# Performance work log

Hardware: AMD Instinct MI355X
Metric: run time of the kernel (lower is better)

Reference implementation:

```python
import jax, jax.numpy as jnp
import numpy as np

D_MODEL = 1024
N_HEADS = 16
D_K = D_MODEL // N_HEADS
SCALE = float(np.sqrt(D_K))


def depthwise3(x, w, b):
    # x: [B, S, D]; w: [D, 3] (PyTorch Conv1d weight [D,1,3] squeezed); b: [D]
    # cross-correlation with kernel_size=3, padding=1, groups=D
    xp = jnp.pad(x, ((0, 0), (1, 1), (0, 0)))
    return xp[:, :-2] * w[:, 0] + xp[:, 1:-1] * w[:, 1] + xp[:, 2:] * w[:, 2] + b


def setup_inputs() -> dict:
    key = jax.random.key(0)
    ks = jax.random.split(key, 16)
    B, S, D = 2, 2048, D_MODEL
    s_lin = 1.0 / np.sqrt(D)
    s_dw = 1.0 / np.sqrt(3)
    inp = {
        "x": jax.random.normal(ks[0], (B, S, D), dtype=jnp.float32),
        "dwq_w": jax.random.uniform(ks[1], (D, 3), jnp.float32, -s_dw, s_dw),
        "dwq_b": jax.random.uniform(ks[2], (D,), jnp.float32, -s_dw, s_dw),
        "dwk_w": jax.random.uniform(ks[3], (D, 3), jnp.float32, -s_dw, s_dw),
        "dwk_b": jax.random.uniform(ks[4], (D,), jnp.float32, -s_dw, s_dw),
        "dwv_w": jax.random.uniform(ks[5], (D, 3), jnp.float32, -s_dw, s_dw),
        "dwv_b": jax.random.uniform(ks[6], (D,), jnp.float32, -s_dw, s_dw),
        "wq": jax.random.uniform(ks[7], (D, D), jnp.float32, -s_lin, s_lin),
        "bq": jax.random.uniform(ks[8], (D,), jnp.float32, -s_lin, s_lin),
        "wk": jax.random.uniform(ks[9], (D, D), jnp.float32, -s_lin, s_lin),
        "bk": jax.random.uniform(ks[10], (D,), jnp.float32, -s_lin, s_lin),
        "wv": jax.random.uniform(ks[11], (D, D), jnp.float32, -s_lin, s_lin),
        "bv": jax.random.uniform(ks[12], (D,), jnp.float32, -s_lin, s_lin),
        "wo": jax.random.uniform(ks[13], (D, D), jnp.float32, -s_lin, s_lin),
        "bo": jax.random.uniform(ks[14], (D,), jnp.float32, -s_lin, s_lin),
    }
    return inp


def reference(x, dwq_w, dwq_b, dwk_w, dwk_b, dwv_w, dwv_b,
              wq, bq, wk, bk, wv, bv, wo, bo):
    B, S, D = x.shape
    # depthwise conv (k=3, pad=1) then linear projection (PyTorch: y = x @ W^T + b)
    q = depthwise3(x, dwq_w, dwq_b) @ wq.T + bq
    k = depthwise3(x, dwk_w, dwk_b) @ wk.T + bk
    v = depthwise3(x, dwv_w, dwv_b) @ wv.T + bv
    # [B, H, S, d_k]
    q = q.reshape(B, S, N_HEADS, D_K).transpose(0, 2, 1, 3)
    k = k.reshape(B, S, N_HEADS, D_K).transpose(0, 2, 1, 3)
    v = v.reshape(B, S, N_HEADS, D_K).transpose(0, 2, 1, 3)
    scores = jnp.einsum("bhqd,bhkd->bhqk", q, k) / SCALE
    attn = jax.nn.softmax(scores, axis=-1)  # dropout=0 (eval)
    out = jnp.einsum("bhqk,bhkd->bhqd", attn, v)
    out = out.transpose(0, 2, 1, 3).reshape(B, S, D)
    return out @ wo.T + bo
```

## Files before the change

kernel.cpp:

```cpp
#include <hip/hip_runtime.h>

typedef __bf16 bf16x8 __attribute__((ext_vector_type(8)));
typedef float f32x4 __attribute__((ext_vector_type(4)));
typedef float f32x16 __attribute__((ext_vector_type(16)));
typedef unsigned short u16x8 __attribute__((ext_vector_type(8)));
typedef unsigned short u16x4 __attribute__((ext_vector_type(4)));
typedef unsigned int u32x2 __attribute__((ext_vector_type(2)));

__device__ __forceinline__ unsigned short f2bf(float f) {
  union { float f; unsigned int u; } v; v.f = f;
  unsigned int r = v.u + 0x7FFFu + ((v.u >> 16) & 1u);
  return (unsigned short)(r >> 16);
}

__device__ __forceinline__ void gload_lds16(const void* g, void* l) {
  __builtin_amdgcn_global_load_lds(
      (const __attribute__((address_space(1))) void*)g,
      (__attribute__((address_space(3))) void*)l, 16, 0, 0);
}

__global__ __launch_bounds__(256)
void conv3_kernel(const float* __restrict__ x,
                  const float* __restrict__ wq, const float* __restrict__ bq,
                  const float* __restrict__ wk, const float* __restrict__ bk,
                  const float* __restrict__ wv, const float* __restrict__ bv,
                  unsigned short* __restrict__ cq, unsigned short* __restrict__ ck,
                  unsigned short* __restrict__ cv)
{
  int t = blockIdx.x;
  int s = t & 2047;
  int d0 = threadIdx.x * 4;
  int base = t * 1024 + d0;
  f32x4 xc = *(const f32x4*)(x + base);
  f32x4 xm = (s > 0)    ? *(const f32x4*)(x + base - 1024) : f32x4{0.f,0.f,0.f,0.f};
  f32x4 xp = (s < 2047) ? *(const f32x4*)(x + base + 1024) : f32x4{0.f,0.f,0.f,0.f};

  #pragma unroll
  for (int path = 0; path < 3; path++) {
    const float* wP = (path == 0) ? wq : ((path == 1) ? wk : wv);
    const float* bP = (path == 0) ? bq : ((path == 1) ? bk : bv);
    unsigned short* oP = (path == 0) ? cq : ((path == 1) ? ck : cv);
    f32x4 w0 = *(const f32x4*)(wP + d0*3);
    f32x4 w1 = *(const f32x4*)(wP + d0*3 + 4);
    f32x4 w2 = *(const f32x4*)(wP + d0*3 + 8);
    f32x4 b4 = *(const f32x4*)(bP + d0);
    u16x4 o;
    #pragma unroll
    for (int dd = 0; dd < 4; dd++) {
      float wa, wb, wc;
      int j0 = dd*3, j1 = dd*3+1, j2 = dd*3+2;
      wa = (j0 < 4) ? w0[j0] : ((j0 < 8) ? w1[j0-4] : w2[j0-8]);
      wb = (j1 < 4) ? w0[j1] : ((j1 < 8) ? w1[j1-4] : w2[j1-8]);
      wc = (j2 < 4) ? w0[j2] : ((j2 < 8) ? w1[j2-4] : w2[j2-8]);
      o[dd] = f2bf(xm[dd]*wa + xc[dd]*wb + xp[dd]*wc + b4[dd]);
    }
    *(u16x4*)(oP + base) = o;
  }
}

__global__ __launch_bounds__(256)
void cvt_w_kernel(const float* __restrict__ w0, const float* __restrict__ w1,
                  const float* __restrict__ w2, const float* __restrict__ w3,
                  unsigned short* __restrict__ o0, unsigned short* __restrict__ o1,
                  unsigned short* __restrict__ o2, unsigned short* __restrict__ o3)
{
  const float* src; unsigned short* dst;
  switch (blockIdx.y) {
    case 0: src = w0; dst = o0; break;
    case 1: src = w1; dst = o1; break;
    case 2: src = w2; dst = o2; break;
    default: src = w3; dst = o3; break;
  }
  int i = blockIdx.x * 1024 + threadIdx.x * 4;
  f32x4 v = *(const f32x4*)(src + i);
  u16x4 o;
  #pragma unroll
  for (int j = 0; j < 4; j++) o[j] = f2bf(v[j]);
  *(u16x4*)(dst + i) = o;
}

__global__ __launch_bounds__(256, 3)
void gemm_qkv_kernel(const unsigned short* __restrict__ cq, const unsigned short* __restrict__ ck,
                     const unsigned short* __restrict__ cv,
                     const unsigned short* __restrict__ wqb, const unsigned short* __restrict__ wkb,
                     const unsigned short* __restrict__ wvb,
                     const float* __restrict__ bq, const float* __restrict__ bk,
                     const float* __restrict__ bv,
                     unsigned short* __restrict__ qo, unsigned short* __restrict__ ko,
                     unsigned short* __restrict__ vtb)
{
  const int K = 1024;
  __shared__ alignas(16) unsigned short lA[3 * 4096];
  __shared__ alignas(16) unsigned short lB[3 * 4096];
  int z = blockIdx.z;
  const unsigned short* A = (z == 0) ? cq : ((z == 1) ? ck : cv);
  const unsigned short* W = (z == 0) ? wqb : ((z == 1) ? wkb : wvb);
  const float* bias       = (z == 0) ? bq : ((z == 1) ? bk : bv);
  float scale             = (z == 0) ? 0.125f * 1.4426950408889634f : 1.0f;

  int bm = blockIdx.y * 128, bn = blockIdx.x * 128;
  const int tid = threadIdx.x, lane = tid & 63, w = tid >> 6;
  const int lrow = lane & 15, lgrp = lane >> 4;
  const int wm = (w >> 1) * 64, wn = (w & 1) * 64;

  f32x4 acc[4][4];
  #pragma unroll
  for (int i = 0; i < 4; i++)
    #pragma unroll
    for (int j = 0; j < 4; j++) acc[i][j] = f32x4{0.f,0.f,0.f,0.f};

  auto STAGE = [&](int buf, int k0) {
    #pragma unroll
    for (int c = 0; c < 2; c++) {
      int slot_base = c * 256 + w * 64;
      int slot = slot_base + lane;
      int row = slot >> 2;
      int kc8 = ((slot & 3) ^ (row & 3)) << 3;
      gload_lds16(A + (size_t)(bm + row) * K + k0 + kc8, lA + buf * 4096 + slot_base * 8);
      gload_lds16(W + (size_t)(bn + row) * K + k0 + kc8, lB + buf * 4096 + slot_base * 8);
    }
  };

  STAGE(0, 0);
  STAGE(1, 32);
  int cur = 0, stg = 2;

  for (int t = 0; t < 32; t++) {
    if (t < 31) { asm volatile("s_waitcnt vmcnt(4)" ::: "memory"); }
    else        { asm volatile("s_waitcnt vmcnt(0)" ::: "memory"); }
    __builtin_amdgcn_s_barrier();
    __builtin_amdgcn_sched_barrier(0);
    if (t + 2 < 32) STAGE(stg, (t + 2) * 32);

    bf16x8 af[4], bfr[4];
    #pragma unroll
    for (int mt = 0; mt < 4; mt++) {
      int rr = wm + mt*16 + lrow;
      af[mt] = *(const bf16x8*)(lA + cur*4096 + (rr << 5) + ((lgrp ^ (rr & 3)) << 3));
    }
    #pragma unroll
    for (int nt = 0; nt < 4; nt++) {
      int rr = wn + nt*16 + lrow;
      bfr[nt] = *(const bf16x8*)(lB + cur*4096 + (rr << 5) + ((lgrp ^ (rr & 3)) << 3));
    }
    #pragma unroll
    for (int mt = 0; mt < 4; mt++)
      #pragma unroll
      for (int nt = 0; nt < 4; nt++)
        acc[mt][nt] = __builtin_amdgcn_mfma_f32_16x16x32_bf16(af[mt], bfr[nt], acc[mt][nt], 0, 0, 0);

    cur = (cur == 2) ? 0 : cur + 1;
    stg = (stg == 2) ? 0 : stg + 1;
  }

  if (z == 2) {
    #pragma unroll
    for (int mt = 0; mt < 4; mt++) {
      #pragma unroll
      for (int nt = 0; nt < 4; nt++) {
        int gn = bn + wn + nt*16 + lrow;
        float bb = bias[gn];
        int h = gn >> 6, dk = gn & 63;
        int gm0 = bm + wm + mt*16 + lgrp*4;
        int b = gm0 >> 11, s0 = gm0 & 2047;
        int tile = s0 >> 6, ckc = (s0 >> 3) & 7, e0 = s0 & 7;
        u16x4 pk;
        #pragma unroll
        for (int i = 0; i < 4; i++) pk[i] = f2bf(acc[mt][nt][i] + bb);
        unsigned short* dst = vtb +
            ((((size_t)(b*16 + h) * 32 + tile) * 8 + ckc) * 64 + dk) * 8 + e0;
        *(u16x4*)dst = pk;
      }
    }
  } else {
    unsigned short* O = (z == 0) ? qo : ko;
    #pragma unroll
    for (int mt = 0; mt < 4; mt++) {
      #pragma unroll
      for (int nt = 0; nt < 4; nt++) {
        int gn = bn + wn + nt*16 + lrow;
        float bb = bias[gn];
        int h = gn >> 6, dk = gn & 63;
        #pragma unroll
        for (int i = 0; i < 4; i++) {
          int gm = bm + wm + mt*16 + lgrp*4 + i;
          int b = gm >> 11, s = gm & 2047;
          float val = (acc[mt][nt][i] + bb) * scale;
          O[((size_t)(b*16 + h) * 2048 + s) * 64 + dk] = f2bf(val);
        }
      }
    }
  }
}

__global__ __launch_bounds__(256)
void gemm_out_kernel(const unsigned short* __restrict__ A, const unsigned short* __restrict__ W,
                     const float* __restrict__ bias, float* __restrict__ Out)
{
  const int K = 1024;
  __shared__ alignas(16) unsigned short lA[3 * 2048];
  __shared__ alignas(16) unsigned short lB[3 * 4096];
  int bm = blockIdx.y * 64, bn = blockIdx.x * 128;
  const int tid = threadIdx.x, lane = tid & 63, w = tid >> 6;
  const int lrow = lane & 15, lgrp = lane >> 4;
  const int wm = (w >> 1) * 32, wn = (w & 1) * 64;

  f32x4 acc[2][4];
  #pragma unroll
  for (int mt = 0; mt < 2; mt++)
    #pragma unroll
    for (int nt = 0; nt < 4; nt++) acc[mt][nt] = f32x4{0.f,0.f,0.f,0.f};

  auto STAGE = [&](int buf, int k0) {
    {
      int slot = tid;
      int row = slot >> 2;
      int kc8 = ((slot & 3) ^ (row & 3)) << 3;
      gload_lds16(A + (size_t)(bm + row) * K + k0 + kc8, lA + buf * 2048 + (w * 64) * 8);
    }
    #pragma unroll
    for (int c = 0; c < 2; c++) {
      int slot_base = c * 256 + w * 64;
      int slot = slot_base + lane;
      int row = slot >> 2;
      int kc8 = ((slot & 3) ^ (row & 3)) << 3;
      gload_lds16(W + (size_t)(bn + row) * K + k0 + kc8, lB + buf * 4096 + slot_base * 8);
    }
  };

  STAGE(0, 0);
  STAGE(1, 32);
  int cur = 0, stg = 2;

  for (int t = 0; t < 32; t++) {
    if (t < 31) { asm volatile("s_waitcnt vmcnt(3)" ::: "memory"); }
    else        { asm volatile("s_waitcnt vmcnt(0)" ::: "memory"); }
    __builtin_amdgcn_s_barrier();
    __builtin_amdgcn_sched_barrier(0);
    if (t + 2 < 32) STAGE(stg, (t + 2) * 32);

    bf16x8 af[2], bfr[4];
    #pragma unroll
    for (int mt = 0; mt < 2; mt++) {
      int rr = wm + mt*16 + lrow;
      af[mt] = *(const bf16x8*)(lA + cur*2048 + (rr << 5) + ((lgrp ^ (rr & 3)) << 3));
    }
    #pragma unroll
    for (int nt = 0; nt < 4; nt++) {
      int rr = wn + nt*16 + lrow;
      bfr[nt] = *(const bf16x8*)(lB + cur*4096 + (rr << 5) + ((lgrp ^ (rr & 3)) << 3));
    }
    #pragma unroll
    for (int mt = 0; mt < 2; mt++)
      #pragma unroll
      for (int nt = 0; nt < 4; nt++)
        acc[mt][nt] = __builtin_amdgcn_mfma_f32_16x16x32_bf16(af[mt], bfr[nt], acc[mt][nt], 0, 0, 0);

    cur = (cur == 2) ? 0 : cur + 1;
    stg = (stg == 2) ? 0 : stg + 1;
  }

  #pragma unroll
  for (int mt = 0; mt < 2; mt++) {
    #pragma unroll
    for (int nt = 0; nt < 4; nt++) {
      int gn = bn + wn + nt*16 + lrow;
      float bb = bias[gn];
      #pragma unroll
      for (int i = 0; i < 4; i++) {
        int gm = bm + wm + mt*16 + lgrp*4 + i;
        Out[(size_t)gm * 1024 + gn] = acc[mt][nt][i] + bb;
      }
    }
  }
}

__global__ __launch_bounds__(256, 2)
void attn_kernel(const unsigned short* __restrict__ Q, const unsigned short* __restrict__ K,
                 const unsigned short* __restrict__ Vtb, unsigned short* __restrict__ O)
{
  const int S = 2048, NT = 32;
  int n = blockIdx.x;
  int xcd = n & 7, r = n >> 3;
  int bh = (xcd << 2) | (r & 3);
  int qbase = (r >> 2) * 128;

  const int tid = threadIdx.x, lane = tid & 63, w = tid >> 6;
  const int lq = lane & 31;
  const int lh = lane >> 5;
  const unsigned short* Qh = Q   + (size_t)bh * S * 64;
  const unsigned short* Kh = K   + (size_t)bh * S * 64;
  const unsigned short* Vh = Vtb + (size_t)bh * 32 * 4096;

  __shared__ alignas(16) unsigned short Kb[3][4096];

  bf16x8 qf[4];
  {
    const unsigned short* qp = Qh + (size_t)(qbase + w*32 + lq) * 64 + lh * 8;
    #pragma unroll
    for (int ks = 0; ks < 4; ks++)
      qf[ks] = *(const bf16x8*)(qp + ks * 16);
  }
  bf16x8 ones;
  {
    union { __bf16 b; unsigned short u; } one; one.u = 0x3F80;
    #pragma unroll
    for (int j = 0; j < 8; j++) ones[j] = one.b;
  }

  f32x16 oacc[2], lacc;
  #pragma unroll
  for (int i = 0; i < 16; i++) { oacc[0][i] = 0.f; oacc[1][i] = 0.f; lacc[i] = 0.f; }

  auto STAGE = [&](int buf, int gt) {
    const unsigned short* gK = Kh + (size_t)gt * 4096;
    #pragma unroll
    for (int c = 0; c < 2; c++) {
      int slot_base = c * 256 + w * 64;
      int slot = slot_base + lane;
      int row = slot >> 3;
      int srcoff = (row << 6) + (((slot & 7) ^ (row & 7)) << 3);
      gload_lds16(gK + srcoff, &Kb[buf][slot_base * 8]);
    }
  };
  auto VLOAD = [&](bf16x8 (&dst)[8], int gt) {
    const unsigned short* gV = Vh + (size_t)gt * 4096;
    #pragma unroll
    for (int kp = 0; kp < 4; kp++)
      #pragma unroll
      for (int dt = 0; dt < 2; dt++)
        dst[kp*2 + dt] = *(const bf16x8*)(gV + (((kp << 1) + lh) << 9) + ((dt*32 + lq) << 3));
  };

  bf16x8 vfA[8], vfB[8];
  VLOAD(vfA, 0);
  STAGE(0, 0);
  STAGE(1, 1);
  int cur = 0, stg = 2;

  auto body = [&](int t, bf16x8 (&vcur)[8], bf16x8 (&vnext)[8]) {
    if (t < NT - 1) { asm volatile("s_waitcnt vmcnt(2)" ::: "memory"); }
    else            { asm volatile("s_waitcnt vmcnt(0)" ::: "memory"); }
    __builtin_amdgcn_s_barrier();
    __builtin_amdgcn_sched_barrier(0);
    if (t + 1 < NT) VLOAD(vnext, t + 1);
    if (t + 2 < NT) STAGE(stg, t + 2);

    f32x16 sacc[2];
    #pragma unroll
    for (int i = 0; i < 16; i++) { sacc[0][i] = 0.f; sacc[1][i] = 0.f; }
    #pragma unroll
    for (int ks = 0; ks < 4; ks++) {
      #pragma unroll
      for (int kt = 0; kt < 2; kt++) {
        int row = kt*32 + lq;
        bf16x8 kf = *(const bf16x8*)(&Kb[cur][(row << 6) + ((((ks<<1)+lh) ^ (row & 7)) << 3)]);
        sacc[kt] = __builtin_amdgcn_mfma_f32_32x32x16_bf16(kf, qf[ks], sacc[kt], 0, 0, 0);
      }
    }

    bf16x8 pa[4];
    #pragma unroll
    for (int kp = 0; kp < 4; kp++) {
      const int sv = kp >> 1;
      const int rb = (kp & 1) * 8;
      float p[8];
      #pragma unroll
      for (int i = 0; i < 8; i++)
        p[i] = __builtin_amdgcn_exp2f(sacc[sv][rb + i]);
      unsigned int X, Y, Z, W2;
      asm("v_cvt_pk_bf16_f32 %0, %1, %2" : "=v"(X)  : "v"(p[0]), "v"(p[1]));
      asm("v_cvt_pk_bf16_f32 %0, %1, %2" : "=v"(Y)  : "v"(p[2]), "v"(p[3]));
      asm("v_cvt_pk_bf16_f32 %0, %1, %2" : "=v"(Z)  : "v"(p[4]), "v"(p[5]));
      asm("v_cvt_pk_bf16_f32 %0, %1, %2" : "=v"(W2) : "v"(p[6]), "v"(p[7]));
      u32x2 rxz = __builtin_amdgcn_permlane32_swap(X, Z, false, false);
      u32x2 ryw = __builtin_amdgcn_permlane32_swap(Y, W2, false, false);
      union { unsigned int u[4]; bf16x8 v; } pk;
      pk.u[0] = rxz[0]; pk.u[1] = ryw[0]; pk.u[2] = rxz[1]; pk.u[3] = ryw[1];
      pa[kp] = pk.v;
    }

    __builtin_amdgcn_s_setprio(1);
    #pragma unroll
    for (int kp = 0; kp < 4; kp++) {
      #pragma unroll
      for (int dt = 0; dt < 2; dt++)
        oacc[dt] = __builtin_amdgcn_mfma_f32_32x32x16_bf16(pa[kp], vcur[kp*2 + dt], oacc[dt], 0, 0, 0);
      lacc = __builtin_amdgcn_mfma_f32_32x32x16_bf16(pa[kp], ones, lacc, 0, 0, 0);
    }
    __builtin_amdgcn_s_setprio(0);

    cur = (cur == 2) ? 0 : cur + 1;
    stg = (stg == 2) ? 0 : stg + 1;
  };

  for (int t = 0; t < NT; t += 2) {
    body(t,     vfA, vfB);
    body(t + 1, vfB, vfA);
  }

  int b = bh >> 4, h = bh & 15;
  #pragma unroll
  for (int reg = 0; reg < 16; reg++) {
    float rl = 1.0f / lacc[reg];
    int qrow = qbase + w*32 + (reg & 3) + 8*(reg >> 2) + 4*lh;
    unsigned short* dst = O + ((size_t)(b*2048 + qrow)) * 1024 + h*64 + lq;
    dst[0]  = f2bf(oacc[0][reg] * rl);
    dst[32] = f2bf(oacc[1][reg] * rl);
  }
}

extern "C" void kernel_launch(void* const* d_in, const int* in_sizes, int n_in,
                              void* d_out, int out_size, void* d_ws, size_t ws_size,
                              hipStream_t stream)
{
  const float* x     = (const float*)d_in[0];
  const float* dwq_w = (const float*)d_in[1];
  const float* dwq_b = (const float*)d_in[2];
  const float* dwk_w = (const float*)d_in[3];
  const float* dwk_b = (const float*)d_in[4];
  const float* dwv_w = (const float*)d_in[5];
  const float* dwv_b = (const float*)d_in[6];
  const float* wq    = (const float*)d_in[7];
  const float* bq    = (const float*)d_in[8];
  const float* wk    = (const float*)d_in[9];
  const float* bk    = (const float*)d_in[10];
  const float* wv    = (const float*)d_in[11];
  const float* bv    = (const float*)d_in[12];
  const float* wo    = (const float*)d_in[13];
  const float* bo    = (const float*)d_in[14];
  float* out = (float*)d_out;

  char* ws = (char*)d_ws;
  const size_t MB = 1024 * 1024;
  unsigned short* cq  = (unsigned short*)(ws + 0);
  unsigned short* ck  = (unsigned short*)(ws + 8*MB);
  unsigned short* cv  = (unsigned short*)(ws + 16*MB);
  unsigned short* qd  = (unsigned short*)(ws + 24*MB);
  unsigned short* kd  = (unsigned short*)(ws + 32*MB);
  unsigned short* wqb = (unsigned short*)(ws + 48*MB);
  unsigned short* wkb = (unsigned short*)(ws + 50*MB);
  unsigned short* wvb = (unsigned short*)(ws + 52*MB);
  unsigned short* wob = (unsigned short*)(ws + 54*MB);
  unsigned short* attn_out = cq;
  unsigned short* vtb      = ck;

  cvt_w_kernel<<<dim3(1024, 4), 256, 0, stream>>>(wq, wk, wv, wo, wqb, wkb, wvb, wob);
  conv3_kernel<<<4096, 256, 0, stream>>>(x, dwq_w, dwq_b, dwk_w, dwk_b, dwv_w, dwv_b, cq, ck, cv);
  gemm_qkv_kernel<<<dim3(8, 32, 3), 256, 0, stream>>>(cq, ck, cv, wqb, wkb, wvb, bq, bk, bv, qd, kd, vtb);
  attn_kernel<<<512, 256, 0, stream>>>(qd, kd, vtb, attn_out);
  gemm_out_kernel<<<dim3(8, 64), 256, 0, stream>>>(attn_out, wob, bo, out);
}
```

Before: 131.4 us.

## Split attention over key halves with combine pass, stage V via LDS, fuse prep kernels

Attention is split into two key-range halves (flash-decoding style), which doubles the grid to 1024 blocks and raises the occupancy hint. A new combine kernel merges the two partial outputs, weighting each by its softmax denominator. The partials are staged in the output buffer. V is now laid out row-major per tile and loaded into LDS with swizzled async loads instead of direct register loads. The weight conversion and conv kernels are fused into one launch. The cost is an extra kernel and round trip through partial buffers, plus more LDS per block.

```diff
diff --git a/kernel.cpp b/kernel.cpp
--- a/kernel.cpp
+++ b/kernel.cpp
@@ -12,6 +12,10 @@
   unsigned int r = v.u + 0x7FFFu + ((v.u >> 16) & 1u);
   return (unsigned short)(r >> 16);
 }
+__device__ __forceinline__ float bf2f(unsigned short h) {
+  union { unsigned int u; float f; } v; v.u = ((unsigned int)h) << 16;
+  return v.f;
+}
 
 __device__ __forceinline__ void gload_lds16(const void* g, void* l) {
   __builtin_amdgcn_global_load_lds(
@@ -20,13 +24,34 @@
 }
 
 __global__ __launch_bounds__(256)
-void conv3_kernel(const float* __restrict__ x,
-                  const float* __restrict__ wq, const float* __restrict__ bq,
-                  const float* __restrict__ wk, const float* __restrict__ bk,
-                  const float* __restrict__ wv, const float* __restrict__ bv,
-                  unsigned short* __restrict__ cq, unsigned short* __restrict__ ck,
-                  unsigned short* __restrict__ cv)
-{
+void prep_kernel(const float* __restrict__ x,
+                 const float* __restrict__ wq3, const float* __restrict__ bq3,
+                 const float* __restrict__ wk3, const float* __restrict__ bk3,
+                 const float* __restrict__ wv3, const float* __restrict__ bv3,
+                 unsigned short* __restrict__ cq, unsigned short* __restrict__ ck,
+                 unsigned short* __restrict__ cv,
+                 const float* __restrict__ wq, const float* __restrict__ wk,
+                 const float* __restrict__ wv, const float* __restrict__ wo,
+                 unsigned short* __restrict__ wqb, unsigned short* __restrict__ wkb,
+                 unsigned short* __restrict__ wvb, unsigned short* __restrict__ wob)
+{
+  if (blockIdx.x >= 4096) {
+    int bb = blockIdx.x - 4096;
+    const float* src; unsigned short* dst;
+    switch (bb >> 10) {
+      case 0: src = wq; dst = wqb; break;
+      case 1: src = wk; dst = wkb; break;
+      case 2: src = wv; dst = wvb; break;
+      default: src = wo; dst = wob; break;
+    }
+    int i = (bb & 1023) * 1024 + threadIdx.x * 4;
+    f32x4 v = *(const f32x4*)(src + i);
+    u16x4 o;
+    #pragma unroll
+    for (int j = 0; j < 4; j++) o[j] = f2bf(v[j]);
+    *(u16x4*)(dst + i) = o;
+    return;
+  }
   int t = blockIdx.x;
   int s = t & 2047;
   int d0 = threadIdx.x * 4;
@@ -37,8 +62,8 @@
 
   #pragma unroll
   for (int path = 0; path < 3; path++) {
-    const float* wP = (path == 0) ? wq : ((path == 1) ? wk : wv);
-    const float* bP = (path == 0) ? bq : ((path == 1) ? bk : bv);
+    const float* wP = (path == 0) ? wq3 : ((path == 1) ? wk3 : wv3);
+    const float* bP = (path == 0) ? bq3 : ((path == 1) ? bk3 : bv3);
     unsigned short* oP = (path == 0) ? cq : ((path == 1) ? ck : cv);
     f32x4 w0 = *(const f32x4*)(wP + d0*3);
     f32x4 w1 = *(const f32x4*)(wP + d0*3 + 4);
@@ -56,27 +81,6 @@
     }
     *(u16x4*)(oP + base) = o;
   }
-}
-
-__global__ __launch_bounds__(256)
-void cvt_w_kernel(const float* __restrict__ w0, const float* __restrict__ w1,
-                  const float* __restrict__ w2, const float* __restrict__ w3,
-                  unsigned short* __restrict__ o0, unsigned short* __restrict__ o1,
-                  unsigned short* __restrict__ o2, unsigned short* __restrict__ o3)
-{
-  const float* src; unsigned short* dst;
-  switch (blockIdx.y) {
-    case 0: src = w0; dst = o0; break;
-    case 1: src = w1; dst = o1; break;
-    case 2: src = w2; dst = o2; break;
-    default: src = w3; dst = o3; break;
-  }
-  int i = blockIdx.x * 1024 + threadIdx.x * 4;
-  f32x4 v = *(const f32x4*)(src + i);
-  u16x4 o;
-  #pragma unroll
-  for (int j = 0; j < 4; j++) o[j] = f2bf(v[j]);
-  *(u16x4*)(dst + i) = o;
 }
 
 __global__ __launch_bounds__(256, 3)
@@ -163,12 +167,11 @@
         int h = gn >> 6, dk = gn & 63;
         int gm0 = bm + wm + mt*16 + lgrp*4;
         int b = gm0 >> 11, s0 = gm0 & 2047;
-        int tile = s0 >> 6, ckc = (s0 >> 3) & 7, e0 = s0 & 7;
         u16x4 pk;
         #pragma unroll
         for (int i = 0; i < 4; i++) pk[i] = f2bf(acc[mt][nt][i] + bb);
         unsigned short* dst = vtb +
-            ((((size_t)(b*16 + h) * 32 + tile) * 8 + ckc) * 64 + dk) * 8 + e0;
+            ((((size_t)(b*16 + h)) * 32 + (s0 >> 6)) * 64 + dk) * 64 + (s0 & 63);
         *(u16x4*)dst = pk;
       }
     }
@@ -275,15 +278,19 @@
   }
 }
 
-__global__ __launch_bounds__(256, 2)
+__global__ __launch_bounds__(256, 4)
 void attn_kernel(const unsigned short* __restrict__ Q, const unsigned short* __restrict__ K,
-                 const unsigned short* __restrict__ Vtb, unsigned short* __restrict__ O)
-{
-  const int S = 2048, NT = 32;
+                 const unsigned short* __restrict__ Vtb,
+                 unsigned short* __restrict__ Opart, float* __restrict__ lbuf)
+{
+  const int S = 2048, NT = 16;
   int n = blockIdx.x;
-  int xcd = n & 7, r = n >> 3;
-  int bh = (xcd << 2) | (r & 3);
-  int qbase = (r >> 2) * 128;
+  int xcd = n & 7, rest = n >> 3;
+  int bh = (xcd << 2) | (rest & 3);
+  int qt = (rest >> 2) & 15;
+  int half = rest >> 6;
+  int qbase = qt * 128;
+  int kt0 = half * 16;
 
   const int tid = threadIdx.x, lane = tid & 63, w = tid >> 6;
   const int lq = lane & 31;
@@ -293,6 +300,7 @@
   const unsigned short* Vh = Vtb + (size_t)bh * 32 * 4096;
 
   __shared__ alignas(16) unsigned short Kb[3][4096];
+  __shared__ alignas(16) unsigned short Vb[2][4096];
 
   bf16x8 qf[4];
   {
@@ -312,7 +320,7 @@
   #pragma unroll
   for (int i = 0; i < 16; i++) { oacc[0][i] = 0.f; oacc[1][i] = 0.f; lacc[i] = 0.f; }
 
-  auto STAGE = [&](int buf, int gt) {
+  auto KSTAGE = [&](int buf, int gt) {
     const unsigned short* gK = Kh + (size_t)gt * 4096;
     #pragma unroll
     for (int c = 0; c < 2; c++) {
@@ -323,28 +331,30 @@
       gload_lds16(gK + srcoff, &Kb[buf][slot_base * 8]);
     }
   };
-  auto VLOAD = [&](bf16x8 (&dst)[8], int gt) {
+  auto VSTAGE = [&](int buf, int gt) {
     const unsigned short* gV = Vh + (size_t)gt * 4096;
     #pragma unroll
-    for (int kp = 0; kp < 4; kp++)
-      #pragma unroll
-      for (int dt = 0; dt < 2; dt++)
-        dst[kp*2 + dt] = *(const bf16x8*)(gV + (((kp << 1) + lh) << 9) + ((dt*32 + lq) << 3));
+    for (int c = 0; c < 2; c++) {
+      int slot_base = c * 256 + w * 64;
+      int slot = slot_base + lane;
+      int row = slot >> 3;
+      int srcoff = (row << 6) + (((slot & 7) ^ (row & 7)) << 3);
+      gload_lds16(gV + srcoff, &Vb[buf][slot_base * 8]);
+    }
   };
 
-  bf16x8 vfA[8], vfB[8];
-  VLOAD(vfA, 0);
-  STAGE(0, 0);
-  STAGE(1, 1);
-  int cur = 0, stg = 2;
-
-  auto body = [&](int t, bf16x8 (&vcur)[8], bf16x8 (&vnext)[8]) {
+  KSTAGE(0, kt0);
+  VSTAGE(0, kt0);
+  KSTAGE(1, kt0 + 1);
+  int kcur = 0, kstg = 2, vcur = 0;
+
+  for (int t = 0; t < NT; t++) {
     if (t < NT - 1) { asm volatile("s_waitcnt vmcnt(2)" ::: "memory"); }
     else            { asm volatile("s_waitcnt vmcnt(0)" ::: "memory"); }
     __builtin_amdgcn_s_barrier();
     __builtin_amdgcn_sched_barrier(0);
-    if (t + 1 < NT) VLOAD(vnext, t + 1);
-    if (t + 2 < NT) STAGE(stg, t + 2);
+    if (t + 1 < NT) VSTAGE(vcur ^ 1, kt0 + t + 1);
+    if (t + 2 < NT) KSTAGE(kstg, kt0 + t + 2);
 
     f32x16 sacc[2];
     #pragma unroll
@@ -354,7 +364,7 @@
       #pragma unroll
       for (int kt = 0; kt < 2; kt++) {
         int row = kt*32 + lq;
-        bf16x8 kf = *(const bf16x8*)(&Kb[cur][(row << 6) + ((((ks<<1)+lh) ^ (row & 7)) << 3)]);
+        bf16x8 kf = *(const bf16x8*)(&Kb[kcur][(row << 6) + ((((ks<<1)+lh) ^ (row & 7)) << 3)]);
         sacc[kt] = __builtin_amdgcn_mfma_f32_32x32x16_bf16(kf, qf[ks], sacc[kt], 0, 0, 0);
       }
     }
@@ -384,30 +394,50 @@
     #pragma unroll
     for (int kp = 0; kp < 4; kp++) {
       #pragma unroll
-      for (int dt = 0; dt < 2; dt++)
-        oacc[dt] = __builtin_amdgcn_mfma_f32_32x32x16_bf16(pa[kp], vcur[kp*2 + dt], oacc[dt], 0, 0, 0);
+      for (int dt = 0; dt < 2; dt++) {
+        int row = dt*32 + lq;
+        bf16x8 vf = *(const bf16x8*)(&Vb[vcur][(row << 6) + ((((kp<<1)+lh) ^ (row & 7)) << 3)]);
+        oacc[dt] = __builtin_amdgcn_mfma_f32_32x32x16_bf16(pa[kp], vf, oacc[dt], 0, 0, 0);
+      }
       lacc = __builtin_amdgcn_mfma_f32_32x32x16_bf16(pa[kp], ones, lacc, 0, 0, 0);
     }
     __builtin_amdgcn_s_setprio(0);
 
-    cur = (cur == 2) ? 0 : cur + 1;
-    stg = (stg == 2) ? 0 : stg + 1;
-  };
-
-  for (int t = 0; t < NT; t += 2) {
-    body(t,     vfA, vfB);
-    body(t + 1, vfB, vfA);
-  }
-
-  int b = bh >> 4, h = bh & 15;
+    kcur = (kcur == 2) ? 0 : kcur + 1;
+    kstg = (kstg == 2) ? 0 : kstg + 1;
+    vcur ^= 1;
+  }
+
   #pragma unroll
   for (int reg = 0; reg < 16; reg++) {
     float rl = 1.0f / lacc[reg];
     int qrow = qbase + w*32 + (reg & 3) + 8*(reg >> 2) + 4*lh;
-    unsigned short* dst = O + ((size_t)(b*2048 + qrow)) * 1024 + h*64 + lq;
-    dst[0]  = f2bf(oacc[0][reg] * rl);
-    dst[32] = f2bf(oacc[1][reg] * rl);
-  }
+    size_t base = ((size_t)(half*32 + bh) * 2048 + qrow) * 64;
+    Opart[base + lq]      = f2bf(oacc[0][reg] * rl);
+    Opart[base + 32 + lq] = f2bf(oacc[1][reg] * rl);
+    if (lq == 0) lbuf[(size_t)half * 65536 + bh * 2048 + qrow] = lacc[reg];
+  }
+}
+
+__global__ __launch_bounds__(256)
+void combine_kernel(const unsigned short* __restrict__ Opart, const float* __restrict__ lbuf,
+                    unsigned short* __restrict__ O)
+{
+  int gid = blockIdx.x * 256 + threadIdx.x;
+  int r = gid >> 3;
+  int d0 = (gid & 7) * 8;
+  float l1 = lbuf[r], l2 = lbuf[65536 + r];
+  float inv = 1.0f / (l1 + l2);
+  float w1 = l1 * inv, w2 = l2 * inv;
+  u16x8 p1 = *(const u16x8*)(Opart + (size_t)r * 64 + d0);
+  u16x8 p2 = *(const u16x8*)(Opart + 4194304 + (size_t)r * 64 + d0);
+  int bh = r >> 11, s = r & 2047;
+  int b = bh >> 4, h = bh & 15;
+  unsigned short* dst = O + ((size_t)(b*2048 + s)) * 1024 + h*64 + d0;
+  u16x8 o;
+  #pragma unroll
+  for (int j = 0; j < 8; j++) o[j] = f2bf(w1 * bf2f(p1[j]) + w2 * bf2f(p2[j]));
+  *(u16x8*)dst = o;
 }
 
 extern "C" void kernel_launch(void* const* d_in, const int* in_sizes, int n_in,
@@ -442,12 +472,15 @@
   unsigned short* wkb = (unsigned short*)(ws + 50*MB);
   unsigned short* wvb = (unsigned short*)(ws + 52*MB);
   unsigned short* wob = (unsigned short*)(ws + 54*MB);
+  float*          lbuf = (float*)(ws + 56*MB);
   unsigned short* attn_out = cq;
   unsigned short* vtb      = ck;
-
-  cvt_w_kernel<<<dim3(1024, 4), 256, 0, stream>>>(wq, wk, wv, wo, wqb, wkb, wvb, wob);
-  conv3_kernel<<<4096, 256, 0, stream>>>(x, dwq_w, dwq_b, dwk_w, dwk_b, dwv_w, dwv_b, cq, ck, cv);
+  unsigned short* opart    = (unsigned short*)d_out;
+
+  prep_kernel<<<8192, 256, 0, stream>>>(x, dwq_w, dwq_b, dwk_w, dwk_b, dwv_w, dwv_b,
+                                        cq, ck, cv, wq, wk, wv, wo, wqb, wkb, wvb, wob);
   gemm_qkv_kernel<<<dim3(8, 32, 3), 256, 0, stream>>>(cq, ck, cv, wqb, wkb, wvb, bq, bk, bv, qd, kd, vtb);
-  attn_kernel<<<512, 256, 0, stream>>>(qd, kd, vtb, attn_out);
+  attn_kernel<<<1024, 256, 0, stream>>>(qd, kd, vtb, opart, lbuf);
+  combine_kernel<<<2048, 256, 0, stream>>>(opart, lbuf, attn_out);
   gemm_out_kernel<<<dim3(8, 64), 256, 0, stream>>>(attn_out, wob, bo, out);
 }
```

New measurement: 133.1 us. Within noise of the previous version (+1.3%).

## Stage V through LDS, sum softmax rows with VALU, merge prep kernels

Applied to the files above, without the earlier changes.

Attention now loads V tiles into a triple-buffered LDS ring alongside K, using the same XOR swizzle and async global-to-LDS loads. The V transpose layout written by the QKV GEMM changes to a plain [dk][s] tile to match. Previously V fragments went straight from global memory into registers. The row-sum MFMA against a ones vector is replaced by VALU adds with a cross-lane shuffle reduction at the end. The weight-conversion and conv kernels are merged into one launch to save a kernel launch. In exchange, attention uses more LDS, which may reduce occupancy, and it adds LDS read traffic.

```diff
diff --git a/kernel.cpp b/kernel.cpp
--- a/kernel.cpp
+++ b/kernel.cpp
@@ -20,13 +20,34 @@
 }
 
 __global__ __launch_bounds__(256)
-void conv3_kernel(const float* __restrict__ x,
-                  const float* __restrict__ wq, const float* __restrict__ bq,
-                  const float* __restrict__ wk, const float* __restrict__ bk,
-                  const float* __restrict__ wv, const float* __restrict__ bv,
-                  unsigned short* __restrict__ cq, unsigned short* __restrict__ ck,
-                  unsigned short* __restrict__ cv)
+void prep_kernel(const float* __restrict__ x,
+                 const float* __restrict__ wq3, const float* __restrict__ bq3,
+                 const float* __restrict__ wk3, const float* __restrict__ bk3,
+                 const float* __restrict__ wv3, const float* __restrict__ bv3,
+                 unsigned short* __restrict__ cq, unsigned short* __restrict__ ck,
+                 unsigned short* __restrict__ cv,
+                 const float* __restrict__ wq, const float* __restrict__ wk,
+                 const float* __restrict__ wv, const float* __restrict__ wo,
+                 unsigned short* __restrict__ wqb, unsigned short* __restrict__ wkb,
+                 unsigned short* __restrict__ wvb, unsigned short* __restrict__ wob)
 {
+  if (blockIdx.x >= 4096) {
+    int bb = blockIdx.x - 4096;
+    const float* src; unsigned short* dst;
+    switch (bb >> 10) {
+      case 0: src = wq; dst = wqb; break;
+      case 1: src = wk; dst = wkb; break;
+      case 2: src = wv; dst = wvb; break;
+      default: src = wo; dst = wob; break;
+    }
+    int i = (bb & 1023) * 1024 + threadIdx.x * 4;
+    f32x4 v = *(const f32x4*)(src + i);
+    u16x4 o;
+    #pragma unroll
+    for (int j = 0; j < 4; j++) o[j] = f2bf(v[j]);
+    *(u16x4*)(dst + i) = o;
+    return;
+  }
   int t = blockIdx.x;
   int s = t & 2047;
   int d0 = threadIdx.x * 4;
@@ -37,8 +58,8 @@
 
   #pragma unroll
   for (int path = 0; path < 3; path++) {
-    const float* wP = (path == 0) ? wq : ((path == 1) ? wk : wv);
-    const float* bP = (path == 0) ? bq : ((path == 1) ? bk : bv);
+    const float* wP = (path == 0) ? wq3 : ((path == 1) ? wk3 : wv3);
+    const float* bP = (path == 0) ? bq3 : ((path == 1) ? bk3 : bv3);
     unsigned short* oP = (path == 0) ? cq : ((path == 1) ? ck : cv);
     f32x4 w0 = *(const f32x4*)(wP + d0*3);
     f32x4 w1 = *(const f32x4*)(wP + d0*3 + 4);
@@ -56,27 +77,6 @@
     }
     *(u16x4*)(oP + base) = o;
   }
-}
-
-__global__ __launch_bounds__(256)
-void cvt_w_kernel(const float* __restrict__ w0, const float* __restrict__ w1,
-                  const float* __restrict__ w2, const float* __restrict__ w3,
-                  unsigned short* __restrict__ o0, unsigned short* __restrict__ o1,
-                  unsigned short* __restrict__ o2, unsigned short* __restrict__ o3)
-{
-  const float* src; unsigned short* dst;
-  switch (blockIdx.y) {
-    case 0: src = w0; dst = o0; break;
-    case 1: src = w1; dst = o1; break;
-    case 2: src = w2; dst = o2; break;
-    default: src = w3; dst = o3; break;
-  }
-  int i = blockIdx.x * 1024 + threadIdx.x * 4;
-  f32x4 v = *(const f32x4*)(src + i);
-  u16x4 o;
-  #pragma unroll
-  for (int j = 0; j < 4; j++) o[j] = f2bf(v[j]);
-  *(u16x4*)(dst + i) = o;
 }
 
 __global__ __launch_bounds__(256, 3)
@@ -163,12 +163,11 @@
         int h = gn >> 6, dk = gn & 63;
         int gm0 = bm + wm + mt*16 + lgrp*4;
         int b = gm0 >> 11, s0 = gm0 & 2047;
-        int tile = s0 >> 6, ckc = (s0 >> 3) & 7, e0 = s0 & 7;
         u16x4 pk;
         #pragma unroll
         for (int i = 0; i < 4; i++) pk[i] = f2bf(acc[mt][nt][i] + bb);
         unsigned short* dst = vtb +
-            ((((size_t)(b*16 + h) * 32 + tile) * 8 + ckc) * 64 + dk) * 8 + e0;
+            ((((size_t)(b*16 + h)) * 32 + (s0 >> 6)) * 64 + dk) * 64 + (s0 & 63);
         *(u16x4*)dst = pk;
       }
     }
@@ -293,6 +292,7 @@
   const unsigned short* Vh = Vtb + (size_t)bh * 32 * 4096;
 
   __shared__ alignas(16) unsigned short Kb[3][4096];
+  __shared__ alignas(16) unsigned short Vb[3][4096];
 
   bf16x8 qf[4];
   {
@@ -301,19 +301,15 @@
     for (int ks = 0; ks < 4; ks++)
       qf[ks] = *(const bf16x8*)(qp + ks * 16);
   }
-  bf16x8 ones;
-  {
-    union { __bf16 b; unsigned short u; } one; one.u = 0x3F80;
-    #pragma unroll
-    for (int j = 0; j < 8; j++) ones[j] = one.b;
-  }
-
-  f32x16 oacc[2], lacc;
-  #pragma unroll
-  for (int i = 0; i < 16; i++) { oacc[0][i] = 0.f; oacc[1][i] = 0.f; lacc[i] = 0.f; }
+
+  f32x16 oacc[2];
+  #pragma unroll
+  for (int i = 0; i < 16; i++) { oacc[0][i] = 0.f; oacc[1][i] = 0.f; }
+  float lsum = 0.f;
 
   auto STAGE = [&](int buf, int gt) {
     const unsigned short* gK = Kh + (size_t)gt * 4096;
+    const unsigned short* gV = Vh + (size_t)gt * 4096;
     #pragma unroll
     for (int c = 0; c < 2; c++) {
       int slot_base = c * 256 + w * 64;
@@ -321,29 +317,20 @@
       int row = slot >> 3;
       int srcoff = (row << 6) + (((slot & 7) ^ (row & 7)) << 3);
       gload_lds16(gK + srcoff, &Kb[buf][slot_base * 8]);
+      gload_lds16(gV + srcoff, &Vb[buf][slot_base * 8]);
     }
   };
-  auto VLOAD = [&](bf16x8 (&dst)[8], int gt) {
-    const unsigned short* gV = Vh + (size_t)gt * 4096;
-    #pragma unroll
-    for (int kp = 0; kp < 4; kp++)
-      #pragma unroll
-      for (int dt = 0; dt < 2; dt++)
-        dst[kp*2 + dt] = *(const bf16x8*)(gV + (((kp << 1) + lh) << 9) + ((dt*32 + lq) << 3));
-  };
-
-  bf16x8 vfA[8], vfB[8];
-  VLOAD(vfA, 0);
+
   STAGE(0, 0);
   STAGE(1, 1);
   int cur = 0, stg = 2;
 
-  auto body = [&](int t, bf16x8 (&vcur)[8], bf16x8 (&vnext)[8]) {
-    if (t < NT - 1) { asm volatile("s_waitcnt vmcnt(2)" ::: "memory"); }
+  for (int t = 0; t < NT; t++) {
+    if (t < NT - 1) { asm volatile("s_waitcnt vmcnt(4)" ::: "memory"); }
     else            { asm volatile("s_waitcnt vmcnt(0)" ::: "memory"); }
     __builtin_amdgcn_s_barrier();
     __builtin_amdgcn_sched_barrier(0);
-    if (t + 1 < NT) VLOAD(vnext, t + 1);
+
     if (t + 2 < NT) STAGE(stg, t + 2);
 
     f32x16 sacc[2];
@@ -368,6 +355,7 @@
       #pragma unroll
       for (int i = 0; i < 8; i++)
         p[i] = __builtin_amdgcn_exp2f(sacc[sv][rb + i]);
+      lsum += ((p[0]+p[1]) + (p[2]+p[3])) + ((p[4]+p[5]) + (p[6]+p[7]));
       unsigned int X, Y, Z, W2;
       asm("v_cvt_pk_bf16_f32 %0, %1, %2" : "=v"(X)  : "v"(p[0]), "v"(p[1]));
       asm("v_cvt_pk_bf16_f32 %0, %1, %2" : "=v"(Y)  : "v"(p[2]), "v"(p[3]));
@@ -384,26 +372,27 @@
     #pragma unroll
     for (int kp = 0; kp < 4; kp++) {
       #pragma unroll
-      for (int dt = 0; dt < 2; dt++)
-        oacc[dt] = __builtin_amdgcn_mfma_f32_32x32x16_bf16(pa[kp], vcur[kp*2 + dt], oacc[dt], 0, 0, 0);
-      lacc = __builtin_amdgcn_mfma_f32_32x32x16_bf16(pa[kp], ones, lacc, 0, 0, 0);
+      for (int dt = 0; dt < 2; dt++) {
+        int row = dt*32 + lq;
+        bf16x8 vf = *(const bf16x8*)(&Vb[cur][(row << 6) + ((((kp<<1)+lh) ^ (row & 7)) << 3)]);
+        oacc[dt] = __builtin_amdgcn_mfma_f32_32x32x16_bf16(pa[kp], vf, oacc[dt], 0, 0, 0);
+      }
     }
     __builtin_amdgcn_s_setprio(0);
 
     cur = (cur == 2) ? 0 : cur + 1;
     stg = (stg == 2) ? 0 : stg + 1;
-  };
-
-  for (int t = 0; t < NT; t += 2) {
-    body(t,     vfA, vfB);
-    body(t + 1, vfB, vfA);
-  }
+  }
+
+  float ltot = lsum + __shfl_xor(lsum, 32, 64);
 
   int b = bh >> 4, h = bh & 15;
   #pragma unroll
   for (int reg = 0; reg < 16; reg++) {
-    float rl = 1.0f / lacc[reg];
-    int qrow = qbase + w*32 + (reg & 3) + 8*(reg >> 2) + 4*lh;
+    int qrl = (reg & 3) + 8*(reg >> 2) + 4*lh;
+    float lq_ = __shfl(ltot, qrl, 64);
+    float rl = 1.0f / lq_;
+    int qrow = qbase + w*32 + qrl;
     unsigned short* dst = O + ((size_t)(b*2048 + qrow)) * 1024 + h*64 + lq;
     dst[0]  = f2bf(oacc[0][reg] * rl);
     dst[32] = f2bf(oacc[1][reg] * rl);
@@ -445,8 +434,8 @@
   unsigned short* attn_out = cq;
   unsigned short* vtb      = ck;
 
-  cvt_w_kernel<<<dim3(1024, 4), 256, 0, stream>>>(wq, wk, wv, wo, wqb, wkb, wvb, wob);
-  conv3_kernel<<<4096, 256, 0, stream>>>(x, dwq_w, dwq_b, dwk_w, dwk_b, dwv_w, dwv_b, cq, ck, cv);
+  prep_kernel<<<8192, 256, 0, stream>>>(x, dwq_w, dwq_b, dwk_w, dwk_b, dwv_w, dwv_b,
+                                        cq, ck, cv, wq, wk, wv, wo, wqb, wkb, wvb, wob);
   gemm_qkv_kernel<<<dim3(8, 32, 3), 256, 0, stream>>>(cq, ck, cv, wqb, wkb, wvb, bq, bk, bv, qd, kd, vtb);
   attn_kernel<<<512, 256, 0, stream>>>(qd, kd, vtb, attn_out);
   gemm_out_kernel<<<dim3(8, 64), 256, 0, stream>>>(attn_out, wob, bo, out);
```

Result: faster. 127.1 us (-3.2%).
